# Kernel optimization log

Hardware: AMD Instinct MI355X
Metric: run time of the kernel (lower is better)

## Reference

```python
import jax, jax.numpy as jnp
import numpy as np

WS = 8       # window_size
SHIFT = 4    # shift_size
NH = 6       # num_heads
C = 192      # dim
EPS = 1e-5


def _rel_index(ws):
    # standard Swin relative position index, [ws*ws, ws*ws]
    coords = np.stack(np.meshgrid(np.arange(ws), np.arange(ws), indexing='ij')).reshape(2, -1)
    rel = coords[:, :, None] - coords[:, None, :]            # [2, N, N]
    rel = rel.transpose(1, 2, 0) + (ws - 1)                  # shift to >= 0
    return rel[..., 0] * (2 * ws - 1) + rel[..., 1]          # [N, N]


def _attn_mask(h, w, ws, shift):
    # shifted-window attention mask, [nW, N, N] with 0 / -100
    img = np.zeros((h, w), dtype=np.float32)
    cnt = 0
    for hs in (slice(0, -ws), slice(-ws, -shift), slice(-shift, None)):
        for wsl in (slice(0, -ws), slice(-ws, -shift), slice(-shift, None)):
            img[hs, wsl] = cnt
            cnt += 1
    mw = img.reshape(h // ws, ws, w // ws, ws).transpose(0, 2, 1, 3).reshape(-1, ws * ws)
    diff = mw[:, None, :] - mw[:, :, None]
    return np.where(diff != 0, -100.0, 0.0).astype(np.float32)


def _ln(x, g, b):
    m = x.mean(-1, keepdims=True)
    v = ((x - m) ** 2).mean(-1, keepdims=True)
    return (x - m) / jnp.sqrt(v + EPS) * g + b


def setup_inputs() -> dict:
    key = jax.random.key(0)
    ks = jax.random.split(key, 16)
    B, H, W = 32, 64, 64
    Ch = 4 * C
    s = 0.02
    return {
        'x': jax.random.normal(ks[0], (B, H * W, C), jnp.float32),
        'h': H,
        'w': W,
        'norm1_g': jnp.ones((C,), jnp.float32),
        'norm1_b': jnp.zeros((C,), jnp.float32),
        'qkv_w': jax.random.normal(ks[1], (3 * C, C), jnp.float32) * s,
        'qkv_b': jnp.zeros((3 * C,), jnp.float32),
        'rpb_table': jax.random.normal(ks[2], ((2 * WS - 1) ** 2, NH), jnp.float32) * s,
        'proj_w': jax.random.normal(ks[3], (C, C), jnp.float32) * s,
        'proj_b': jnp.zeros((C,), jnp.float32),
        'norm2_g': jnp.ones((C,), jnp.float32),
        'norm2_b': jnp.zeros((C,), jnp.float32),
        'fc1_w': jax.random.normal(ks[4], (Ch, C), jnp.float32) * s,
        'fc1_b': jnp.zeros((Ch,), jnp.float32),
        'fc2_w': jax.random.normal(ks[5], (C, Ch), jnp.float32) * s,
        'fc2_b': jnp.zeros((C,), jnp.float32),
    }


def reference(x, h, w, norm1_g, norm1_b, qkv_w, qkv_b, rpb_table, proj_w, proj_b,
              norm2_g, norm2_b, fc1_w, fc1_b, fc2_w, fc2_b):
    B, L, _ = x.shape
    N = WS * WS
    hd = C // NH
    scale = hd ** -0.5
    nW = (h // WS) * (w // WS)

    shortcut = x
    xn = _ln(x, norm1_g, norm1_b).reshape(B, h, w, C)
    xs = jnp.roll(xn, (-SHIFT, -SHIFT), (1, 2))
    # window partition -> [B*nW, N, C]
    xw = xs.reshape(B, h // WS, WS, w // WS, WS, C).transpose(0, 1, 3, 2, 4, 5).reshape(-1, N, C)

    qkv = (xw @ qkv_w.T + qkv_b).reshape(-1, N, 3, NH, hd).transpose(2, 0, 3, 1, 4)
    q, k, v = qkv[0], qkv[1], qkv[2]                          # [B*nW, NH, N, hd]
    attn = jnp.einsum('whnd,whmd->whnm', q * scale, k)        # [B*nW, NH, N, N]
    bias = rpb_table[jnp.asarray(_rel_index(WS))].transpose(2, 0, 1)  # [NH, N, N]
    attn = attn + bias[None]
    mask = jnp.asarray(_attn_mask(h, w, WS, SHIFT))           # [nW, N, N]
    attn = attn.reshape(B, nW, NH, N, N) + mask[None, :, None]
    attn = jax.nn.softmax(attn.reshape(-1, NH, N, N), axis=-1)
    out = jnp.einsum('whnm,whmd->whnd', attn, v).transpose(0, 2, 1, 3).reshape(-1, N, C)
    out = out @ proj_w.T + proj_b

    # window reverse + unroll
    out = out.reshape(B, h // WS, w // WS, WS, WS, C).transpose(0, 1, 3, 2, 4, 5).reshape(B, h, w, C)
    out = jnp.roll(out, (SHIFT, SHIFT), (1, 2)).reshape(B, h * w, C)

    x = shortcut + out
    xn = _ln(x, norm2_g, norm2_b)
    mlp = jax.nn.gelu(xn @ fc1_w.T + fc1_b, approximate=False) @ fc2_w.T + fc2_b
    return x + mlp
```

## Files before the change

kernel.cpp:

```cpp
#include <hip/hip_runtime.h>
#include <hip/hip_bf16.h>
#include <math.h>

typedef __bf16 bf16;
typedef __bf16 bf16x4 __attribute__((ext_vector_type(4)));
typedef __bf16 bf16x8 __attribute__((ext_vector_type(8)));
typedef float f32x4 __attribute__((ext_vector_type(4)));

typedef const __attribute__((address_space(1))) char gchar;
typedef __attribute__((address_space(3))) char lchar;

#define BATCH 32
#define HW 64
#define L 4096
#define CDIM 192
#define NHEADS 6
#define HD 32
#define NTOK 131072
#define QKVC 576
#define CH 768

__device__ __forceinline__ int srcrow_of(int row) {
  int win = row >> 6, n = row & 63;
  int bb = win >> 6, wid = win & 63;
  int i = ((wid >> 3) << 3) + (n >> 3);
  int j = ((wid & 7) << 3) + (n & 7);
  return bb * L + ((i + 4) & 63) * HW + ((j + 4) & 63);
}

template <bool PERM, typename TIN>
__global__ __launch_bounds__(256) void ln_kernel(const TIN* __restrict__ xin,
                                                 const float* __restrict__ g,
                                                 const float* __restrict__ bta,
                                                 bf16* __restrict__ yout) {
  int wave = threadIdx.x >> 6;
  int lane = threadIdx.x & 63;
  int tok = blockIdx.x * 4 + wave;
  int src = PERM ? srcrow_of(tok) : tok;
  const TIN* sp = xin + (size_t)src * CDIM;
  float v0 = (float)sp[lane];
  float v1 = (float)sp[lane + 64];
  float v2 = (float)sp[lane + 128];
  float s = v0 + v1 + v2;
#pragma unroll
  for (int off = 32; off; off >>= 1) s += __shfl_xor(s, off, 64);
  float mean = s * (1.0f / 192.0f);
  float d0 = v0 - mean, d1 = v1 - mean, d2 = v2 - mean;
  float q = d0 * d0 + d1 * d1 + d2 * d2;
#pragma unroll
  for (int off = 32; off; off >>= 1) q += __shfl_xor(q, off, 64);
  float rstd = rsqrtf(q * (1.0f / 192.0f) + 1e-5f);
  bf16* dp = yout + (size_t)tok * CDIM;
  dp[lane]       = (bf16)(d0 * rstd * g[lane]       + bta[lane]);
  dp[lane + 64]  = (bf16)(d1 * rstd * g[lane + 64]  + bta[lane + 64]);
  dp[lane + 128] = (bf16)(d2 * rstd * g[lane + 128] + bta[lane + 128]);
}

template <int EPI, typename TR, typename TO>
__global__ __launch_bounds__(256) void gemm_bt(const bf16* __restrict__ A,
                                               const float* __restrict__ W,
                                               const float* __restrict__ bias,
                                               const TR* __restrict__ res,
                                               TO* __restrict__ Cout,
                                               int M, int N, int K, int ldw) {
  __shared__ alignas(16) bf16 As[128 * 32];
  __shared__ alignas(16) bf16 Bs[64 * 32];
  const int gx = gridDim.x;
  const int nb = gx * gridDim.y;
  const int id = blockIdx.y * gx + blockIdx.x;
  const int per = nb >> 3;
  const int jj = ((id & 7) * per) + (id >> 3);
  const int n0 = (jj % gx) * 64;
  const int m0 = (jj / gx) * 128;
  const int tid = threadIdx.x;
  const int lane = tid & 63;
  const int wave = tid >> 6;
  const int wm = (wave >> 1) * 64;
  const int wn = (wave & 1) * 32;
  const int lr = lane & 15;
  const int quad = lane >> 4;

  f32x4 acc[4][2];
#pragma unroll
  for (int i = 0; i < 4; i++)
#pragma unroll
    for (int j = 0; j < 2; j++) acc[i][j] = (f32x4){0.f, 0.f, 0.f, 0.f};

  const int arow = tid >> 2;
  const int akq = (tid & 3) * 8;

  for (int k0 = 0; k0 < K; k0 += 32) {
    const bf16* Ap = A + (size_t)(m0 + arow) * K + k0 + akq;
    *(uint4*)(&As[arow * 32 + akq]) = *(const uint4*)Ap;
    *(uint4*)(&As[(arow + 64) * 32 + akq]) = *(const uint4*)(Ap + (size_t)64 * K);
    const float* Wp = W + (size_t)(n0 + arow) * ldw + k0 + akq;
    float4 w0 = *(const float4*)Wp;
    float4 w1 = *(const float4*)(Wp + 4);
    bf16x8 bw;
    bw[0] = (bf16)w0.x; bw[1] = (bf16)w0.y; bw[2] = (bf16)w0.z; bw[3] = (bf16)w0.w;
    bw[4] = (bf16)w1.x; bw[5] = (bf16)w1.y; bw[6] = (bf16)w1.z; bw[7] = (bf16)w1.w;
    *(bf16x8*)(&Bs[arow * 32 + akq]) = bw;
    __syncthreads();

    bf16x8 af[4], bfr[2];
#pragma unroll
    for (int mi = 0; mi < 4; mi++)
      af[mi] = *(const bf16x8*)(&As[(wm + mi * 16 + lr) * 32 + quad * 8]);
#pragma unroll
    for (int nj = 0; nj < 2; nj++)
      bfr[nj] = *(const bf16x8*)(&Bs[(wn + nj * 16 + lr) * 32 + quad * 8]);
#pragma unroll
    for (int mi = 0; mi < 4; mi++)
#pragma unroll
      for (int nj = 0; nj < 2; nj++)
        acc[mi][nj] = __builtin_amdgcn_mfma_f32_16x16x32_bf16(af[mi], bfr[nj],
                                                              acc[mi][nj], 0, 0, 0);
    __syncthreads();
  }

#pragma unroll
  for (int mi = 0; mi < 4; mi++) {
#pragma unroll
    for (int nj = 0; nj < 2; nj++) {
      int col = n0 + wn + nj * 16 + lr;
      float bv = bias[col];
#pragma unroll
      for (int r = 0; r < 4; r++) {
        int row = m0 + wm + mi * 16 + quad * 4 + r;
        float v = acc[mi][nj][r] + bv;
        size_t didx;
        if (EPI == 3) {
          didx = ((size_t)srcrow_of(row)) * (size_t)N + col;
          v += (float)res[didx];
        } else {
          didx = (size_t)row * N + col;
        }
        Cout[didx] = (TO)v;
      }
    }
  }
}

__device__ __forceinline__ int region64(int h) {
  return (h < 56) ? 0 : ((h < 60) ? 1 : 2);
}

__global__ __launch_bounds__(64) void attn_kernel(const bf16* __restrict__ qkv,
                                                  const float* __restrict__ rpb,
                                                  bf16* __restrict__ out) {
  __shared__ alignas(16) bf16 QKP[64 * 64];
  __shared__ alignas(16) bf16 Vt[32 * 64];
  bf16* Qs = QKP;
  bf16* Ks = QKP + 64 * 32;
  bf16* Ps = QKP;
  const int win = blockIdx.x;
  const int head = blockIdx.y;
  const int lane = threadIdx.x;
  const int lr = lane & 15;
  const int quad = lane >> 4;
  const int wid = win & 63;
  const int wi = wid >> 3, wj = wid & 7;

  const bf16* base = qkv + (size_t)win * 64 * QKVC + head * HD;
#pragma unroll
  for (int rep = 0; rep < 4; rep++) {
    int r = (lane >> 2) + rep * 16;
    int c = (lane & 3) * 8;
    *(uint4*)(&Qs[r * 32 + c]) = *(const uint4*)(base + (size_t)r * QKVC + c);
    *(uint4*)(&Ks[r * 32 + c]) = *(const uint4*)(base + CDIM + (size_t)r * QKVC + c);
    uint4 vv = *(const uint4*)(base + 2 * CDIM + (size_t)r * QKVC + c);
    bf16x8 v8 = __builtin_bit_cast(bf16x8, vv);
#pragma unroll
    for (int j = 0; j < 8; j++) Vt[(c + j) * 64 + r] = v8[j];
  }
  __syncthreads();

  f32x4 s[4][4];
  {
    bf16x8 qf[4], kf[4];
#pragma unroll
    for (int mi = 0; mi < 4; mi++)
      qf[mi] = *(const bf16x8*)(&Qs[(mi * 16 + lr) * 32 + quad * 8]);
#pragma unroll
    for (int nj = 0; nj < 4; nj++)
      kf[nj] = *(const bf16x8*)(&Ks[(nj * 16 + lr) * 32 + quad * 8]);
#pragma unroll
    for (int mi = 0; mi < 4; mi++)
#pragma unroll
      for (int nj = 0; nj < 4; nj++)
        s[mi][nj] = __builtin_amdgcn_mfma_f32_16x16x32_bf16(
            qf[mi], kf[nj], (f32x4){0.f, 0.f, 0.f, 0.f}, 0, 0, 0);
  }

  const float scale = 0.17677669529663687f;
#pragma unroll
  for (int mi = 0; mi < 4; mi++) {
#pragma unroll
    for (int nj = 0; nj < 4; nj++) {
#pragma unroll
      for (int r = 0; r < 4; r++) {
        int rr = mi * 16 + quad * 4 + r;
        int cc = nj * 16 + lr;
        int qi = rr >> 3, qj = rr & 7, ki = cc >> 3, kj = cc & 7;
        int idx = (qi - ki + 7) * 15 + (qj - kj + 7);
        float bv = rpb[idx * NHEADS + head];
        int regr = 3 * region64(wi * 8 + qi) + region64(wj * 8 + qj);
        int regc = 3 * region64(wi * 8 + ki) + region64(wj * 8 + kj);
        float mv = (regr != regc) ? -100.0f : 0.0f;
        s[mi][nj][r] = s[mi][nj][r] * scale + bv + mv;
      }
    }
  }

#pragma unroll
  for (int mi = 0; mi < 4; mi++) {
#pragma unroll
    for (int r = 0; r < 4; r++) {
      float mx = s[mi][0][r];
#pragma unroll
      for (int nj = 1; nj < 4; nj++) mx = fmaxf(mx, s[mi][nj][r]);
#pragma unroll
      for (int off = 1; off < 16; off <<= 1) mx = fmaxf(mx, __shfl_xor(mx, off, 64));
      float sum = 0.f;
#pragma unroll
      for (int nj = 0; nj < 4; nj++) {
        float p = __expf(s[mi][nj][r] - mx);
        s[mi][nj][r] = p;
        sum += p;
      }
#pragma unroll
      for (int off = 1; off < 16; off <<= 1) sum += __shfl_xor(sum, off, 64);
      float inv = 1.0f / sum;
#pragma unroll
      for (int nj = 0; nj < 4; nj++) s[mi][nj][r] *= inv;
    }
  }

#pragma unroll
  for (int mi = 0; mi < 4; mi++)
#pragma unroll
    for (int nj = 0; nj < 4; nj++)
#pragma unroll
      for (int r = 0; r < 4; r++)
        Ps[(mi * 16 + quad * 4 + r) * 64 + nj * 16 + lr] = (bf16)s[mi][nj][r];
  __syncthreads();

  f32x4 o[4][2];
#pragma unroll
  for (int mi = 0; mi < 4; mi++)
#pragma unroll
    for (int nj = 0; nj < 2; nj++) o[mi][nj] = (f32x4){0.f, 0.f, 0.f, 0.f};
#pragma unroll
  for (int ks = 0; ks < 2; ks++) {
    bf16x8 pf[4], vf[2];
#pragma unroll
    for (int mi = 0; mi < 4; mi++)
      pf[mi] = *(const bf16x8*)(&Ps[(mi * 16 + lr) * 64 + ks * 32 + quad * 8]);
#pragma unroll
    for (int nj = 0; nj < 2; nj++)
      vf[nj] = *(const bf16x8*)(&Vt[(nj * 16 + lr) * 64 + ks * 32 + quad * 8]);
#pragma unroll
    for (int mi = 0; mi < 4; mi++)
#pragma unroll
      for (int nj = 0; nj < 2; nj++)
        o[mi][nj] = __builtin_amdgcn_mfma_f32_16x16x32_bf16(pf[mi], vf[nj],
                                                            o[mi][nj], 0, 0, 0);
  }

#pragma unroll
  for (int mi = 0; mi < 4; mi++)
#pragma unroll
    for (int nj = 0; nj < 2; nj++)
#pragma unroll
      for (int r = 0; r < 4; r++) {
        size_t row = (size_t)win * 64 + mi * 16 + quad * 4 + r;
        int col = head * HD + nj * 16 + lr;
        out[row * CDIM + col] = (bf16)o[mi][nj][r];
      }
}

__global__ __launch_bounds__(256) void wconv_kernel(const float* __restrict__ fc1w,
                                                    const float* __restrict__ fc2w,
                                                    bf16* __restrict__ W1b,
                                                    bf16* __restrict__ W2b) {
  int i = blockIdx.x * 256 + threadIdx.x;
  {
    int h = i / 192;
    int cc = i - h * 192;
    int gs = cc >> 3, e = cc & 7;
    int g = (gs & ~7) | ((gs & 7) ^ (h & 7));
    W1b[i] = (bf16)fc1w[h * 192 + g * 8 + e];
  }
  {
    int c = i / 12288;
    int rem = i - c * 12288;
    int n = rem >> 6;
    int cc = rem & 63;
    int gs = cc >> 3, e = cc & 7;
    int g = gs ^ (n & 7);
    W2b[i] = (bf16)fc2w[n * 768 + c * 64 + g * 8 + e];
  }
}

__global__ __launch_bounds__(512, 4) void mlp_fused(
    const bf16* __restrict__ X1,
    const float* __restrict__ g2,
    const float* __restrict__ bt2,
    const bf16* __restrict__ W1b,
    const bf16* __restrict__ W2b,
    const float* __restrict__ b1,
    const float* __restrict__ b2,
    float* __restrict__ out) {
  __shared__ alignas(16) bf16 W1s[64 * 192];
  __shared__ alignas(16) bf16 W2s[192 * 64];
  __shared__ alignas(16) bf16 Hs[8][16 * 64];
  __shared__ float Gs[192], Bn[192];

  const int tid = threadIdx.x;
  const int lane = tid & 63;
  const int wave = tid >> 6;
  const int lr = lane & 15;
  const int quad = lane >> 4;
  const int m0 = blockIdx.x * 128;
  const int arow = m0 + wave * 16 + lr;

  if (tid < 192) { Gs[tid] = g2[tid]; Bn[tid] = bt2[tid]; }
  __syncthreads();

  bf16x8 xr[6];
  {
    const bf16* xp = X1 + (size_t)arow * CDIM + quad * 8;
#pragma unroll
    for (int ks = 0; ks < 6; ks++) xr[ks] = *(const bf16x8*)(xp + ks * 32);
  }
  float s1 = 0.f, s2 = 0.f;
#pragma unroll
  for (int ks = 0; ks < 6; ks++)
#pragma unroll
    for (int j = 0; j < 8; j++) {
      float v = (float)xr[ks][j];
      s1 += v;
      s2 = fmaf(v, v, s2);
    }
  s1 += __shfl_xor(s1, 16, 64); s1 += __shfl_xor(s1, 32, 64);
  s2 += __shfl_xor(s2, 16, 64); s2 += __shfl_xor(s2, 32, 64);
  float mean = s1 * (1.0f / 192.0f);
  float var = fmaxf(s2 * (1.0f / 192.0f) - mean * mean, 0.0f);
  float rstd = rsqrtf(var + 1e-5f);
  bf16x8 aF[6];
#pragma unroll
  for (int ks = 0; ks < 6; ks++) {
    int cb = ks * 32 + quad * 8;
    bf16x8 a;
#pragma unroll
    for (int j = 0; j < 8; j++)
      a[j] = (bf16)(((float)xr[ks][j] - mean) * rstd * Gs[cb + j] + Bn[cb + j]);
    aF[ks] = a;
  }

  f32x4 oacc[12];
#pragma unroll
  for (int nt = 0; nt < 12; nt++) oacc[nt] = (f32x4){0.f, 0.f, 0.f, 0.f};

  for (int c = 0; c < 12; c++) {
    const int h0 = c * 64;
    {
      const size_t cb = (size_t)c * 24576;
      const int off = wave * 1024 + lane * 16;
      const char* gp1 = (const char*)W1b + cb + off;
      const char* gp2 = (const char*)W2b + cb + off;
      char* l1 = (char*)W1s + wave * 1024;
      char* l2 = (char*)W2s + wave * 1024;
#pragma unroll
      for (int i = 0; i < 3; i++) {
        __builtin_amdgcn_global_load_lds((gchar*)(gp1 + i * 8192),
                                         (lchar*)(l1 + i * 8192), 16, 0, 0);
        __builtin_amdgcn_global_load_lds((gchar*)(gp2 + i * 8192),
                                         (lchar*)(l2 + i * 8192), 16, 0, 0);
      }
    }
    __syncthreads();

    f32x4 hacc[4];
#pragma unroll
    for (int hj = 0; hj < 4; hj++) hacc[hj] = (f32x4){0.f, 0.f, 0.f, 0.f};
#pragma unroll
    for (int ks = 0; ks < 6; ks++) {
      int c8 = ks * 4 + quad;
      int base = (c8 & ~7) | ((c8 & 7) ^ (lr & 7));
#pragma unroll
      for (int hj = 0; hj < 4; hj++) {
        bf16x8 wf = *(const bf16x8*)(&W1s[(hj * 16 + lr) * 192 + base * 8]);
        hacc[hj] = __builtin_amdgcn_mfma_f32_16x16x32_bf16(wf, aF[ks], hacc[hj], 0, 0, 0);
      }
    }

#pragma unroll
    for (int hj = 0; hj < 4; hj++) {
      float4 bh4 = *(const float4*)(&b1[h0 + hj * 16 + quad * 4]);
      float bhv[4] = {bh4.x, bh4.y, bh4.z, bh4.w};
      bf16x4 pk;
#pragma unroll
      for (int r = 0; r < 4; r++) {
        float h = hacc[hj][r] + bhv[r];
        float x = fabsf(h) * 0.70710678118654752f;
        float t = __fdividef(1.0f, fmaf(0.3275911f, x, 1.0f));
        float p = t * (0.254829592f +
                  t * (-0.284496736f +
                  t * (1.421413741f +
                  t * (-1.453152027f + t * 1.061405429f))));
        float er = fmaf(-p, __expf(-x * x), 1.0f);
        er = copysignf(er, h);
        pk[r] = (bf16)(0.5f * h * (1.0f + er));
      }
      int gw = (hj * 4 + quad) ^ ((lr & 7) << 1);
      *(bf16x4*)(&Hs[wave][lr * 64 + gw * 4]) = pk;
    }

#pragma unroll
    for (int ks = 0; ks < 2; ks++) {
      int gr = (ks * 8 + quad * 2) ^ ((lr & 7) << 1);
      bf16x8 hF = *(const bf16x8*)(&Hs[wave][lr * 64 + gr * 4]);
      int c8 = ks * 4 + quad;
      int c8s = c8 ^ (lr & 7);
#pragma unroll
      for (int nt = 0; nt < 12; nt++) {
        bf16x8 wF = *(const bf16x8*)(&W2s[(nt * 16 + lr) * 64 + c8s * 8]);
        oacc[nt] = __builtin_amdgcn_mfma_f32_16x16x32_bf16(hF, wF, oacc[nt], 0, 0, 0);
      }
    }
    __syncthreads();
  }

#pragma unroll
  for (int nt = 0; nt < 12; nt++) {
    float fb = b2[nt * 16 + lr];
#pragma unroll
    for (int r = 0; r < 4; r++) {
      size_t row = (size_t)(m0 + wave * 16 + quad * 4 + r);
      size_t idx = row * CDIM + nt * 16 + lr;
      out[idx] = oacc[nt][r] + fb + (float)X1[idx];
    }
  }
}

extern "C" void kernel_launch(void* const* d_in, const int* in_sizes, int n_in,
                              void* d_out, int out_size, void* d_ws, size_t ws_size,
                              hipStream_t stream) {
  const float* x      = (const float*)d_in[0];
  const float* n1g    = (const float*)d_in[3];
  const float* n1b    = (const float*)d_in[4];
  const float* qkv_w  = (const float*)d_in[5];
  const float* qkv_b  = (const float*)d_in[6];
  const float* rpb    = (const float*)d_in[7];
  const float* proj_w = (const float*)d_in[8];
  const float* proj_b = (const float*)d_in[9];
  const float* n2g    = (const float*)d_in[10];
  const float* n2b    = (const float*)d_in[11];
  const float* fc1_w  = (const float*)d_in[12];
  const float* fc1_b  = (const float*)d_in[13];
  const float* fc2_w  = (const float*)d_in[14];
  const float* fc2_b  = (const float*)d_in[15];
  float* out = (float*)d_out;

  char* wsb = (char*)d_ws;
  bf16* Q   = (bf16*)wsb;
  bf16* X1  = (bf16*)wsb;
  bf16* W1b = (bf16*)(wsb + 52428800ull);
  bf16* W2b = (bf16*)(wsb + 52428800ull + 294912ull);
  bf16* T   = (bf16*)(wsb + 150994944ull);

  ln_kernel<true, float><<<32768, 256, 0, stream>>>(x, n1g, n1b, T);
  gemm_bt<0, float, bf16><<<dim3(9, 1024), 256, 0, stream>>>(
      T, qkv_w, qkv_b, nullptr, Q, NTOK, QKVC, CDIM, CDIM);
  attn_kernel<<<dim3(2048, 6), 64, 0, stream>>>(Q, rpb, T);
  gemm_bt<3, float, bf16><<<dim3(3, 1024), 256, 0, stream>>>(
      T, proj_w, proj_b, x, X1, NTOK, CDIM, CDIM, CDIM);
  wconv_kernel<<<576, 256, 0, stream>>>(fc1_w, fc2_w, W1b, W2b);
  mlp_fused<<<1024, 512, 0, stream>>>(X1, n2g, n2b, W1b, W2b, fc1_b, fc2_b, out);
}
```

Before: 541.8 us.

## Double-buffer MLP weight chunks in LDS with smaller hidden slices

Splits the hidden dimension of the fused MLP into 24 slices of 32 instead of 12 of 64. The fc1 and fc2 weight tiles are double-buffered in LDS, and the next slice is prefetched with global_load_lds while the current one is computed. Loads are split by wave: half the waves fetch fc1 and half fetch fc2. The fc2 weight pre-swizzle and the hidden-activation swizzle are changed to match the new 32-wide layout. The aim is to hide weight-load latency behind MFMA work, at the cost of twice as many barriers and less MFMA work per iteration.

```diff
diff --git a/kernel.cpp b/kernel.cpp
--- a/kernel.cpp
+++ b/kernel.cpp
@@ -292,13 +292,14 @@
     W1b[i] = (bf16)fc1w[h * 192 + g * 8 + e];
   }
   {
-    int c = i / 12288;
-    int rem = i - c * 12288;
-    int n = rem >> 6;
-    int cc = rem & 63;
-    int gs = cc >> 3, e = cc & 7;
-    int g = gs ^ (n & 7);
-    W2b[i] = (bf16)fc2w[n * 768 + c * 64 + g * 8 + e];
+    int c = i / 6144;
+    int rem = i - c * 6144;
+    int n = rem >> 5;
+    int cc = rem & 31;
+    int p = cc >> 3;
+    int e = cc & 7;
+    int g = p ^ ((n >> 1) & 3);
+    W2b[i] = (bf16)fc2w[n * 768 + c * 32 + g * 8 + e];
   }
 }
 
@@ -311,9 +312,9 @@
     const float* __restrict__ b1,
     const float* __restrict__ b2,
     float* __restrict__ out) {
-  __shared__ alignas(16) bf16 W1s[64 * 192];
-  __shared__ alignas(16) bf16 W2s[192 * 64];
-  __shared__ alignas(16) bf16 Hs[8][16 * 64];
+  __shared__ alignas(16) bf16 W1s[2][32 * 192];
+  __shared__ alignas(16) bf16 W2s[2][192 * 32];
+  __shared__ alignas(16) bf16 Hs[8][16 * 32];
   __shared__ float Gs[192], Bn[192];
 
   const int tid = threadIdx.x;
@@ -324,7 +325,27 @@
   const int m0 = blockIdx.x * 128;
   const int arow = m0 + wave * 16 + lr;
 
+  auto stage = [&](int c, int b) {
+    const int off = (wave & 3) * 3072 + lane * 16;
+    if (wave < 4) {
+      const char* gp = (const char*)W1b + (size_t)c * 12288 + off;
+      char* lp = (char*)(&W1s[b][0]) + off;
+#pragma unroll
+      for (int i = 0; i < 3; i++)
+        __builtin_amdgcn_global_load_lds((gchar*)(gp + i * 1024),
+                                         (lchar*)(lp + i * 1024), 16, 0, 0);
+    } else {
+      const char* gp = (const char*)W2b + (size_t)c * 12288 + off;
+      char* lp = (char*)(&W2s[b][0]) + off;
+#pragma unroll
+      for (int i = 0; i < 3; i++)
+        __builtin_amdgcn_global_load_lds((gchar*)(gp + i * 1024),
+                                         (lchar*)(lp + i * 1024), 16, 0, 0);
+    }
+  };
+
   if (tid < 192) { Gs[tid] = g2[tid]; Bn[tid] = bt2[tid]; }
+  stage(0, 0);
   __syncthreads();
 
   bf16x8 xr[6];
@@ -362,41 +383,27 @@
 #pragma unroll
   for (int nt = 0; nt < 12; nt++) oacc[nt] = (f32x4){0.f, 0.f, 0.f, 0.f};
 
-  for (int c = 0; c < 12; c++) {
-    const int h0 = c * 64;
-    {
-      const size_t cb = (size_t)c * 24576;
-      const int off = wave * 1024 + lane * 16;
-      const char* gp1 = (const char*)W1b + cb + off;
-      const char* gp2 = (const char*)W2b + cb + off;
-      char* l1 = (char*)W1s + wave * 1024;
-      char* l2 = (char*)W2s + wave * 1024;
-#pragma unroll
-      for (int i = 0; i < 3; i++) {
-        __builtin_amdgcn_global_load_lds((gchar*)(gp1 + i * 8192),
-                                         (lchar*)(l1 + i * 8192), 16, 0, 0);
-        __builtin_amdgcn_global_load_lds((gchar*)(gp2 + i * 8192),
-                                         (lchar*)(l2 + i * 8192), 16, 0, 0);
-      }
-    }
-    __syncthreads();
-
-    f32x4 hacc[4];
-#pragma unroll
-    for (int hj = 0; hj < 4; hj++) hacc[hj] = (f32x4){0.f, 0.f, 0.f, 0.f};
+  int cur = 0;
+  for (int c = 0; c < 24; c++) {
+    if (c < 23) stage(c + 1, cur ^ 1);
+    const int h0 = c * 32;
+
+    f32x4 hacc[2];
+    hacc[0] = (f32x4){0.f, 0.f, 0.f, 0.f};
+    hacc[1] = (f32x4){0.f, 0.f, 0.f, 0.f};
 #pragma unroll
     for (int ks = 0; ks < 6; ks++) {
       int c8 = ks * 4 + quad;
       int base = (c8 & ~7) | ((c8 & 7) ^ (lr & 7));
 #pragma unroll
-      for (int hj = 0; hj < 4; hj++) {
-        bf16x8 wf = *(const bf16x8*)(&W1s[(hj * 16 + lr) * 192 + base * 8]);
+      for (int hj = 0; hj < 2; hj++) {
+        bf16x8 wf = *(const bf16x8*)(&W1s[cur][(hj * 16 + lr) * 192 + base * 8]);
         hacc[hj] = __builtin_amdgcn_mfma_f32_16x16x32_bf16(wf, aF[ks], hacc[hj], 0, 0, 0);
       }
     }
 
 #pragma unroll
-    for (int hj = 0; hj < 4; hj++) {
+    for (int hj = 0; hj < 2; hj++) {
       float4 bh4 = *(const float4*)(&b1[h0 + hj * 16 + quad * 4]);
       float bhv[4] = {bh4.x, bh4.y, bh4.z, bh4.w};
       bf16x4 pk;
@@ -413,23 +420,24 @@
         er = copysignf(er, h);
         pk[r] = (bf16)(0.5f * h * (1.0f + er));
       }
-      int gw = (hj * 4 + quad) ^ ((lr & 7) << 1);
-      *(bf16x4*)(&Hs[wave][lr * 64 + gw * 4]) = pk;
-    }
-
-#pragma unroll
-    for (int ks = 0; ks < 2; ks++) {
-      int gr = (ks * 8 + quad * 2) ^ ((lr & 7) << 1);
-      bf16x8 hF = *(const bf16x8*)(&Hs[wave][lr * 64 + gr * 4]);
-      int c8 = ks * 4 + quad;
-      int c8s = c8 ^ (lr & 7);
+      int g = hj * 4 + quad;
+      int p8 = g ^ (lr & 6);
+      *(bf16x4*)(&Hs[wave][lr * 32 + p8 * 4]) = pk;
+    }
+
+    {
+      int p2 = (quad * 2) ^ (lr & 6);
+      bf16x8 hF = *(const bf16x8*)(&Hs[wave][lr * 32 + p2 * 4]);
+      int key = (lr >> 1) & 3;
 #pragma unroll
       for (int nt = 0; nt < 12; nt++) {
-        bf16x8 wF = *(const bf16x8*)(&W2s[(nt * 16 + lr) * 64 + c8s * 8]);
+        int p = quad ^ key;
+        bf16x8 wF = *(const bf16x8*)(&W2s[cur][(nt * 16 + lr) * 32 + p * 8]);
         oacc[nt] = __builtin_amdgcn_mfma_f32_16x16x32_bf16(hF, wF, oacc[nt], 0, 0, 0);
       }
     }
     __syncthreads();
+    cur ^= 1;
   }
 
 #pragma unroll
```

Measured after the change: 524.1 us. 3.3% less time.
